# Performance work log

Hardware: AMD Instinct MI355X
Metric: run time of the kernel (lower is better)

Reference implementation:

```python
import jax, jax.numpy as jnp
import numpy as np

T, B, F = 256, 128, 1600
H1, H2, H3 = 60, 15, 10   # MLP dims
GH = 5                    # GRU hidden size


def setup_inputs() -> dict:
    key = jax.random.key(0)
    ks = jax.random.split(key, 24)
    s = 0.1
    inp = {
        "X":   jax.random.normal(ks[0], (T, B, F), jnp.float32),
        "W1":  jax.random.normal(ks[1], (H1, F), jnp.float32) * s,
        "b1":  jax.random.normal(ks[2], (H1,), jnp.float32) * s,
        "W2":  jax.random.normal(ks[3], (H2, H1), jnp.float32) * s,
        "b2":  jax.random.normal(ks[4], (H2,), jnp.float32) * s,
        "W3":  jax.random.normal(ks[5], (H3, H2), jnp.float32) * s,
        "b3":  jax.random.normal(ks[6], (H3,), jnp.float32) * s,
    }
    in_sizes = [H3, GH, GH]
    k = 7
    for l in range(3):
        inp[f"w_ih{l}"] = jax.random.normal(ks[k], (3 * GH, in_sizes[l]), jnp.float32) * s; k += 1
        inp[f"w_hh{l}"] = jax.random.normal(ks[k], (3 * GH, GH), jnp.float32) * s; k += 1
        inp[f"b_ih{l}"] = jax.random.normal(ks[k], (3 * GH,), jnp.float32) * s; k += 1
        inp[f"b_hh{l}"] = jax.random.normal(ks[k], (3 * GH,), jnp.float32) * s; k += 1
    inp["Wout"] = jax.random.normal(ks[k], (1, GH), jnp.float32) * s; k += 1
    inp["bout"] = jax.random.normal(ks[k], (1,), jnp.float32) * s
    return inp


def _gru_layer(x, w_ih, w_hh, b_ih, b_hh):
    # x: (Bb, Tt, I). Precompute input-side gates for all timesteps.
    gi = jnp.einsum('bti,gi->btg', x, w_ih) + b_ih  # (Bb, Tt, 3H)

    def step(h_prev, gi_t):
        gh = h_prev @ w_hh.T + b_hh                 # (Bb, 3H)
        ir, iz, in_ = jnp.split(gi_t, 3, axis=-1)
        hr, hz, hn = jnp.split(gh, 3, axis=-1)
        r = jax.nn.sigmoid(ir + hr)
        z = jax.nn.sigmoid(iz + hz)
        n = jnp.tanh(in_ + r * hn)
        h = (1.0 - z) * n + z * h_prev
        return h, h

    h0 = jnp.zeros((x.shape[0], w_hh.shape[1]), x.dtype)
    _, ys = jax.lax.scan(step, h0, jnp.swapaxes(gi, 0, 1))  # (Tt, Bb, H)
    return jnp.swapaxes(ys, 0, 1)                            # (Bb, Tt, H)


def reference(X, W1, b1, W2, b2, W3, b3,
              w_ih0, w_hh0, b_ih0, b_hh0,
              w_ih1, w_hh1, b_ih1, b_hh1,
              w_ih2, w_hh2, b_ih2, b_hh2,
              Wout, bout):
    x = jnp.transpose(X, (1, 0, 2))        # (B, T, 1600): GRU batch_first layout
    h = jnp.tanh(x @ W1.T + b1)
    h = jnp.tanh(h @ W2.T + b2)
    h = h @ W3.T + b3                      # (B, T, 10) -- no activation after last MLP layer
    seq = h
    for p in ((w_ih0, w_hh0, b_ih0, b_hh0),
              (w_ih1, w_hh1, b_ih1, b_hh1),
              (w_ih2, w_hh2, b_ih2, b_hh2)):
        seq = _gru_layer(seq, *p)          # (B, T, 5)
    y = jnp.swapaxes(seq, 0, 1)            # (T, B, 5)
    y = y @ Wout.T + bout                  # (T, B, 1)
    return jnp.swapaxes(y, -1, -2)         # (T, 1, B)
```

## Files before the change

### kernel.cpp

```cpp
#include <hip/hip_runtime.h>
#include <hip/hip_bf16.h>


#define T_DIM 256
#define B_DIM 128
#define F_DIM 1600
#define H1_DIM 60
#define H2_DIM 15
#define H3_DIM 10
#define GH 5
#define NSTEP 50
#define CT 32
#define NCH (T_DIM / CT)

#define DPP_SHR5  0x115
#define DPP_SHR10 0x11A

typedef __attribute__((ext_vector_type(8))) short bf16x8;
typedef __attribute__((ext_vector_type(4))) float f32x4;

__device__ __forceinline__ float fast_tanh(float x) {
    float e = __expf(2.0f * x);
    return 1.0f - __fdividef(2.0f, e + 1.0f);
}
__device__ __forceinline__ float fast_sigmoid(float x) {
    return __fdividef(1.0f, 1.0f + __expf(-x));
}
__device__ __forceinline__ ushort f2bf_rn(float x) {
    uint u = __float_as_uint(x);
    u += 0x7fffu + ((u >> 16) & 1u);
    return (ushort)(u >> 16);
}
template <int CTRL>
__device__ __forceinline__ float dppf(float v) {
    return __int_as_float(
        __builtin_amdgcn_mov_dpp(__float_as_int(v), CTRL, 0xf, 0xf, true));
}
__device__ __forceinline__ float bperm(int addr, float v) {
    return __int_as_float(__builtin_amdgcn_ds_bpermute(addr, __float_as_int(v)));
}

__global__ __launch_bounds__(256) void pack_w1_kernel(
    const float* __restrict__ W1, ushort* __restrict__ Wp)
{
    const int s  = blockIdx.x;
    const int t  = threadIdx.x;
    const int nf = t >> 6;
    const int l  = t & 63;
    const int n  = nf * 16 + (l & 15);
    const int g  = l >> 4;

    ushort hi[8], lo[8];
#pragma unroll
    for (int j = 0; j < 8; ++j) {
        const int k = s * 32 + g * 8 + j;
        const float v = (n < H1_DIM) ? W1[n * F_DIM + k] : 0.0f;
        const ushort h = f2bf_rn(v);
        const float hf = __uint_as_float(((uint)h) << 16);
        const float r  = v - hf;
        hi[j] = h;
        lo[j] = (ushort)(__float_as_uint(r) >> 16);
    }
    ushort* dst = Wp + ((size_t)(s * 8 + nf * 2)) * 512 + l * 8;
#pragma unroll
    for (int j = 0; j < 8; ++j) dst[j] = hi[j];
#pragma unroll
    for (int j = 0; j < 8; ++j) dst[512 + j] = lo[j];
}

__global__ __launch_bounds__(256) void mlp_kernel(
    const float* __restrict__ X,
    const ushort* __restrict__ Wp,
    const float* __restrict__ b1,
    const float* __restrict__ W2, const float* __restrict__ b2,
    const float* __restrict__ W3, const float* __restrict__ b3,
    const float* __restrict__ wih0, const float* __restrict__ bih0,
    float* __restrict__ gi0)
{
    __shared__ float red[4][2048];

    const int tid  = threadIdx.x;
    const int l    = tid & 63;
    const int w    = __builtin_amdgcn_readfirstlane(tid >> 6);
    const int lm   = l & 15;
    const int g    = l >> 4;
    const int row0 = blockIdx.x * 32;

    f32x4 acc[2][4];
#pragma unroll
    for (int mf = 0; mf < 2; ++mf)
#pragma unroll
        for (int nf = 0; nf < 4; ++nf)
            acc[mf][nf] = (f32x4){0.f, 0.f, 0.f, 0.f};

    const int s0 = (w * NSTEP) >> 2;
    const int s1 = ((w + 1) * NSTEP) >> 2;

    float4 x0[2], x1[2];
#pragma unroll
    for (int mf = 0; mf < 2; ++mf) {
        const float* ap = X + (size_t)(row0 + mf * 16 + lm) * F_DIM + s0 * 32 + g * 8;
        x0[mf] = *(const float4*)ap;
        x1[mf] = *(const float4*)(ap + 4);
    }

    for (int s = s0; s < s1; ++s) {
        float4 n0[2], n1[2];
#pragma unroll
        for (int mf = 0; mf < 2; ++mf) {
            n0[mf] = make_float4(0.f, 0.f, 0.f, 0.f);
            n1[mf] = n0[mf];
        }
        if (s + 1 < s1) {
#pragma unroll
            for (int mf = 0; mf < 2; ++mf) {
                const float* ap = X + (size_t)(row0 + mf * 16 + lm) * F_DIM
                                + (s + 1) * 32 + g * 8;
                n0[mf] = *(const float4*)ap;
                n1[mf] = *(const float4*)(ap + 4);
            }
        }
        bf16x8 bh[4], bl[4];
        const ushort* wp_s = Wp + (size_t)s * 4096 + l * 8;
#pragma unroll
        for (int nf = 0; nf < 4; ++nf) {
            bh[nf] = *(const bf16x8*)(wp_s + (nf * 2 + 0) * 512);
            bl[nf] = *(const bf16x8*)(wp_s + (nf * 2 + 1) * 512);
        }
#pragma unroll
        for (int mf = 0; mf < 2; ++mf) {
            const float xs8[8] = {x0[mf].x, x0[mf].y, x0[mf].z, x0[mf].w,
                                  x1[mf].x, x1[mf].y, x1[mf].z, x1[mf].w};
            bf16x8 ah, al;
#pragma unroll
            for (int j = 0; j < 8; ++j) {
                const float v = xs8[j];
                const uint  u = __float_as_uint(v);
                const uint uh = (u + 0x7fffu + ((u >> 16) & 1u)) & 0xffff0000u;
                const float hf = __uint_as_float(uh);
                const float r  = v - hf;
                ah[j] = (short)(uh >> 16);
                al[j] = (short)(__float_as_uint(r) >> 16);
            }
#pragma unroll
            for (int nf = 0; nf < 4; ++nf) {
                f32x4 c = acc[mf][nf];
                c = __builtin_amdgcn_mfma_f32_16x16x32_bf16(al, bh[nf], c, 0, 0, 0);
                c = __builtin_amdgcn_mfma_f32_16x16x32_bf16(ah, bl[nf], c, 0, 0, 0);
                c = __builtin_amdgcn_mfma_f32_16x16x32_bf16(ah, bh[nf], c, 0, 0, 0);
                acc[mf][nf] = c;
            }
        }
#pragma unroll
        for (int mf = 0; mf < 2; ++mf) { x0[mf] = n0[mf]; x1[mf] = n1[mf]; }
    }

    float* myred = &red[w][0];
#pragma unroll
    for (int mf = 0; mf < 2; ++mf)
#pragma unroll
        for (int nf = 0; nf < 4; ++nf)
#pragma unroll
            for (int q = 0; q < 4; ++q)
                myred[(mf * 16 + g * 4 + q) * 64 + nf * 16 + lm] = acc[mf][nf][q];
    __syncthreads();

    float rsum[8];
#pragma unroll
    for (int i = 0; i < 8; ++i) {
        const int p = tid + 256 * i;
        rsum[i] = red[0][p] + red[1][p] + red[2][p] + red[3][p];
    }
    __syncthreads();
    float* redp = &red[2][0];
#pragma unroll
    for (int i = 0; i < 8; ++i) {
        const int p = tid + 256 * i;
        redp[(p >> 6) * 65 + (p & 63)] = rsum[i];
    }
    __syncthreads();
    if (w != 0 || l >= 32) return;

    float h1v[H1_DIM];
#pragma unroll
    for (int o = 0; o < H1_DIM; ++o)
        h1v[o] = fast_tanh(redp[l * 65 + o] + b1[o]);

    float h2v[H2_DIM];
#pragma unroll
    for (int j = 0; j < H2_DIM; ++j) {
        float sacc = b2[j];
#pragma unroll
        for (int o = 0; o < H1_DIM; ++o) sacc += W2[j * H1_DIM + o] * h1v[o];
        h2v[j] = fast_tanh(sacc);
    }

    float h3v[H3_DIM];
#pragma unroll
    for (int m = 0; m < H3_DIM; ++m) {
        float sacc = b3[m];
#pragma unroll
        for (int j = 0; j < H2_DIM; ++j) sacc += W3[m * H2_DIM + j] * h2v[j];
        h3v[m] = sacc;
    }

    float gv[15];
#pragma unroll
    for (int q = 0; q < 15; ++q) {
        float sacc = bih0[q];
#pragma unroll
        for (int m = 0; m < H3_DIM; ++m) sacc += wih0[q * H3_DIM + m] * h3v[m];
        gv[q] = sacc;
    }

    const int row = row0 + l;
    float4* dst = (float4*)(gi0 + (size_t)row * 16);
    dst[0] = make_float4(gv[0],  gv[1],  gv[2],  gv[3]);
    dst[1] = make_float4(gv[4],  gv[5],  gv[6],  gv[7]);
    dst[2] = make_float4(gv[8],  gv[9],  gv[10], gv[11]);
    dst[3] = make_float4(gv[12], gv[13], gv[14], 0.0f);
}


#define STAGE(C) do {                                                       \
    const int _cb = (C) & 1;                                                \
    float4 _v0, _v1;                                                        \
    {                                                                       \
        const int _t = lane >> 2, _q = lane & 3;                            \
        _v0 = *(const float4*)(gi0 +                                        \
            ((size_t)(((C) * CT + _t) * B_DIM + b)) * 16 + _q * 4);         \
    }                                                                       \
    {                                                                       \
        const int _f = lane + 64, _t = _f >> 2, _q = _f & 3;                \
        _v1 = *(const float4*)(gi0 +                                        \
            ((size_t)(((C) * CT + _t) * B_DIM + b)) * 16 + _q * 4);         \
    }                                                                       \
    *(float4*)&gbuf[_cb][lane >> 2][(lane & 3) * 4] = _v0;                  \
    *(float4*)&gbuf[_cb][(lane + 64) >> 2][((lane + 64) & 3) * 4] = _v1;    \
} while (0)

#define PREF(CB, TL) do { pre = lptr[(CB) * (CT * 16) + (TL) * 16]; } while (0)

#define GSTEP(S, PREFCODE) do {                                             \
         \
    float aA = bA + pre;                                                    \
    _Pragma("unroll") for (int _j = 0; _j < GH; ++_j)                       \
        aA = fmaf(wi[_j], xn[_j], aA);                                      \
    float aB = fmaf(wh[0], hn[0], bB);                                      \
    _Pragma("unroll") for (int _j = 1; _j < GH; ++_j)                       \
        aB = fmaf(wh[_j], hn[_j], aB);                                      \
    PREFCODE                                                                \
    const float sAv = aA + aB;                                              \
    const float sg  = fast_sigmoid(sAv);                                    \
    const float rn  = dppf<DPP_SHR10>(sg);        \
    const float zn  = dppf<DPP_SHR5>(sg);         \
    if (lane == 48 && (unsigned)((S) - 3) < (unsigned)T_DIM)                \
        out[((S) - 3) * B_DIM + b] = sAv;    \
    const float nv = fast_tanh(fmaf(rn, aB, aA));                           \
    const float hu = fmaf(zn, hm - nv, nv);                                 \
    const bool _valid = (unsigned)((S) - row) < (unsigned)T_DIM;            \
    hm = _valid ? hu : hm;                                                  \
                  \
    _Pragma("unroll") for (int _j = 0; _j < GH; ++_j) {                     \
        hn[_j] = bperm(a_self[_j], hm);                                     \
        xn[_j] = bperm(a_prev[_j], hm);                                     \
    }                                                                       \
} while (0)

__global__ __launch_bounds__(128, 1) void gru_kernel(
    const float* __restrict__ gi0,
    const float* __restrict__ whh0, const float* __restrict__ bhh0,
    const float* __restrict__ wih1, const float* __restrict__ whh1,
    const float* __restrict__ bih1, const float* __restrict__ bhh1,
    const float* __restrict__ wih2, const float* __restrict__ whh2,
    const float* __restrict__ bih2, const float* __restrict__ bhh2,
    const float* __restrict__ Wout, const float* __restrict__ bout,
    float* __restrict__ out)
{
    __shared__ float gbuf[2][CT][16];

    const int tid  = threadIdx.x;
    const int w    = __builtin_amdgcn_readfirstlane(tid >> 6);
    const int lane = tid & 63;
    const int b    = blockIdx.x;

    if (w == 1) {
        STAGE(0);
        __syncthreads();
        for (int c = 0; c < NCH; ++c) {
            if (c + 1 < NCH) STAGE(c + 1);
            __syncthreads();
        }
        return;
    }

    const int row = lane >> 4;
    const int g   = lane & 15;

    float wi[GH], wh[GH];
    float bA = 0.f, bB = 0.f;
#pragma unroll
    for (int j = 0; j < GH; ++j) { wi[j] = 0.f; wh[j] = 0.f; }

    if (row == 0) {
        if (g < 15) {
#pragma unroll
            for (int j = 0; j < GH; ++j) wh[j] = whh0[g * GH + j];
            bB = bhh0[g];
        }
    } else if (row < 3) {
        const float* wip = (row == 1) ? wih1 : wih2;
        const float* whp = (row == 1) ? whh1 : whh2;
        const float* bip = (row == 1) ? bih1 : bih2;
        const float* bhp = (row == 1) ? bhh1 : bhh2;
        if (g < 15) {
#pragma unroll
            for (int j = 0; j < GH; ++j) {
                wi[j] = wip[g * GH + j];
                wh[j] = whp[g * GH + j];
            }
            bA = bip[g];
            bB = bhp[g];
        }
    } else if (g == 0) {
#pragma unroll
        for (int j = 0; j < GH; ++j) wi[j] = Wout[j];
        bA = bout[0];
    }

    int a_self[GH], a_prev[GH];
    const int sbase = row * 16;
    const int pbase = ((row + 3) & 3) * 16;
#pragma unroll
    for (int j = 0; j < GH; ++j) {
        a_self[j] = (sbase + 10 + j) << 2;
        a_prev[j] = (pbase + 10 + j) << 2;
    }

    const float* lptr = &gbuf[0][0][(row == 0) ? g : 15];

    float hn[GH] = {0.f, 0.f, 0.f, 0.f, 0.f};
    float xn[GH] = {0.f, 0.f, 0.f, 0.f, 0.f};
    float hm = 0.f, pre = 0.f;

    __syncthreads();
    PREF(0, 0);

    for (int c = 0; c < NCH; ++c) {
        const int cb = c & 1;
#pragma unroll 2
        for (int tl = 0; tl < CT; ++tl) {
            const int s = c * CT + tl;
            GSTEP(s, if (tl + 1 < CT) { PREF(cb, tl + 1); });
        }
        __syncthreads();
        if (c + 1 < NCH) { PREF((c + 1) & 1, 0); }
    }

    for (int s = T_DIM; s < T_DIM + 3; ++s) {
        GSTEP(s, ;);
    }
}

extern "C" void kernel_launch(void* const* d_in, const int* in_sizes, int n_in,
                              void* d_out, int out_size, void* d_ws, size_t ws_size,
                              hipStream_t stream)
{
    (void)in_sizes; (void)n_in; (void)out_size; (void)ws_size;

    const float* X    = (const float*)d_in[0];
    const float* W1   = (const float*)d_in[1];
    const float* b1   = (const float*)d_in[2];
    const float* W2   = (const float*)d_in[3];
    const float* b2   = (const float*)d_in[4];
    const float* W3   = (const float*)d_in[5];
    const float* b3   = (const float*)d_in[6];
    const float* wih0 = (const float*)d_in[7];
    const float* whh0 = (const float*)d_in[8];
    const float* bih0 = (const float*)d_in[9];
    const float* bhh0 = (const float*)d_in[10];
    const float* wih1 = (const float*)d_in[11];
    const float* whh1 = (const float*)d_in[12];
    const float* bih1 = (const float*)d_in[13];
    const float* bhh1 = (const float*)d_in[14];
    const float* wih2 = (const float*)d_in[15];
    const float* whh2 = (const float*)d_in[16];
    const float* bih2 = (const float*)d_in[17];
    const float* bhh2 = (const float*)d_in[18];
    const float* Wout = (const float*)d_in[19];
    const float* bout = (const float*)d_in[20];

    ushort* Wp  = (ushort*)d_ws;
    float*  gi0 = (float*)((char*)d_ws + 524288);

    pack_w1_kernel<<<NSTEP, 256, 0, stream>>>(W1, Wp);
    mlp_kernel<<<1024, 256, 0, stream>>>(X, Wp, b1, W2, b2, W3, b3, wih0, bih0, gi0);
    gru_kernel<<<128, 128, 0, stream>>>(gi0, whh0, bhh0,
                                        wih1, whh1, bih1, bhh1,
                                        wih2, whh2, bih2, bhh2,
                                        Wout, bout, (float*)d_out);
}
```

Measured before the change: 112.3 us.

## Fuse MLP and GRU kernels with per-chunk atomic counters for overlap

Merges the MLP producer kernel and the GRU recurrence into one launch. The first 128 blocks run the GRU and spin on a global counter per 32-timestep chunk, while the remaining 1024 blocks run the MLP and bump that chunk's counter when they finish. The aim is to start the serial GRU on early timesteps while later MLP tiles are still computing, hiding the recurrence behind the bandwidth-heavy MLP. This relies on the GRU blocks being co-resident with the producer blocks and adds spin-wait traffic plus a memset launch. The GRU blocks now use 256 threads, so two idle waves only join barriers.

```diff
diff --git a/kernel.cpp b/kernel.cpp
--- a/kernel.cpp
+++ b/kernel.cpp
@@ -12,6 +12,7 @@
 #define NSTEP 50
 #define CT 32
 #define NCH (T_DIM / CT)
+#define NGRU 128
 
 #define DPP_SHR5  0x115
 #define DPP_SHR10 0x11A
@@ -67,177 +68,6 @@
 #pragma unroll
     for (int j = 0; j < 8; ++j) dst[512 + j] = lo[j];
 }
-
-__global__ __launch_bounds__(256) void mlp_kernel(
-    const float* __restrict__ X,
-    const ushort* __restrict__ Wp,
-    const float* __restrict__ b1,
-    const float* __restrict__ W2, const float* __restrict__ b2,
-    const float* __restrict__ W3, const float* __restrict__ b3,
-    const float* __restrict__ wih0, const float* __restrict__ bih0,
-    float* __restrict__ gi0)
-{
-    __shared__ float red[4][2048];
-
-    const int tid  = threadIdx.x;
-    const int l    = tid & 63;
-    const int w    = __builtin_amdgcn_readfirstlane(tid >> 6);
-    const int lm   = l & 15;
-    const int g    = l >> 4;
-    const int row0 = blockIdx.x * 32;
-
-    f32x4 acc[2][4];
-#pragma unroll
-    for (int mf = 0; mf < 2; ++mf)
-#pragma unroll
-        for (int nf = 0; nf < 4; ++nf)
-            acc[mf][nf] = (f32x4){0.f, 0.f, 0.f, 0.f};
-
-    const int s0 = (w * NSTEP) >> 2;
-    const int s1 = ((w + 1) * NSTEP) >> 2;
-
-    float4 x0[2], x1[2];
-#pragma unroll
-    for (int mf = 0; mf < 2; ++mf) {
-        const float* ap = X + (size_t)(row0 + mf * 16 + lm) * F_DIM + s0 * 32 + g * 8;
-        x0[mf] = *(const float4*)ap;
-        x1[mf] = *(const float4*)(ap + 4);
-    }
-
-    for (int s = s0; s < s1; ++s) {
-        float4 n0[2], n1[2];
-#pragma unroll
-        for (int mf = 0; mf < 2; ++mf) {
-            n0[mf] = make_float4(0.f, 0.f, 0.f, 0.f);
-            n1[mf] = n0[mf];
-        }
-        if (s + 1 < s1) {
-#pragma unroll
-            for (int mf = 0; mf < 2; ++mf) {
-                const float* ap = X + (size_t)(row0 + mf * 16 + lm) * F_DIM
-                                + (s + 1) * 32 + g * 8;
-                n0[mf] = *(const float4*)ap;
-                n1[mf] = *(const float4*)(ap + 4);
-            }
-        }
-        bf16x8 bh[4], bl[4];
-        const ushort* wp_s = Wp + (size_t)s * 4096 + l * 8;
-#pragma unroll
-        for (int nf = 0; nf < 4; ++nf) {
-            bh[nf] = *(const bf16x8*)(wp_s + (nf * 2 + 0) * 512);
-            bl[nf] = *(const bf16x8*)(wp_s + (nf * 2 + 1) * 512);
-        }
-#pragma unroll
-        for (int mf = 0; mf < 2; ++mf) {
-            const float xs8[8] = {x0[mf].x, x0[mf].y, x0[mf].z, x0[mf].w,
-                                  x1[mf].x, x1[mf].y, x1[mf].z, x1[mf].w};
-            bf16x8 ah, al;
-#pragma unroll
-            for (int j = 0; j < 8; ++j) {
-                const float v = xs8[j];
-                const uint  u = __float_as_uint(v);
-                const uint uh = (u + 0x7fffu + ((u >> 16) & 1u)) & 0xffff0000u;
-                const float hf = __uint_as_float(uh);
-                const float r  = v - hf;
-                ah[j] = (short)(uh >> 16);
-                al[j] = (short)(__float_as_uint(r) >> 16);
-            }
-#pragma unroll
-            for (int nf = 0; nf < 4; ++nf) {
-                f32x4 c = acc[mf][nf];
-                c = __builtin_amdgcn_mfma_f32_16x16x32_bf16(al, bh[nf], c, 0, 0, 0);
-                c = __builtin_amdgcn_mfma_f32_16x16x32_bf16(ah, bl[nf], c, 0, 0, 0);
-                c = __builtin_amdgcn_mfma_f32_16x16x32_bf16(ah, bh[nf], c, 0, 0, 0);
-                acc[mf][nf] = c;
-            }
-        }
-#pragma unroll
-        for (int mf = 0; mf < 2; ++mf) { x0[mf] = n0[mf]; x1[mf] = n1[mf]; }
-    }
-
-    float* myred = &red[w][0];
-#pragma unroll
-    for (int mf = 0; mf < 2; ++mf)
-#pragma unroll
-        for (int nf = 0; nf < 4; ++nf)
-#pragma unroll
-            for (int q = 0; q < 4; ++q)
-                myred[(mf * 16 + g * 4 + q) * 64 + nf * 16 + lm] = acc[mf][nf][q];
-    __syncthreads();
-
-    float rsum[8];
-#pragma unroll
-    for (int i = 0; i < 8; ++i) {
-        const int p = tid + 256 * i;
-        rsum[i] = red[0][p] + red[1][p] + red[2][p] + red[3][p];
-    }
-    __syncthreads();
-    float* redp = &red[2][0];
-#pragma unroll
-    for (int i = 0; i < 8; ++i) {
-        const int p = tid + 256 * i;
-        redp[(p >> 6) * 65 + (p & 63)] = rsum[i];
-    }
-    __syncthreads();
-    if (w != 0 || l >= 32) return;
-
-    float h1v[H1_DIM];
-#pragma unroll
-    for (int o = 0; o < H1_DIM; ++o)
-        h1v[o] = fast_tanh(redp[l * 65 + o] + b1[o]);
-
-    float h2v[H2_DIM];
-#pragma unroll
-    for (int j = 0; j < H2_DIM; ++j) {
-        float sacc = b2[j];
-#pragma unroll
-        for (int o = 0; o < H1_DIM; ++o) sacc += W2[j * H1_DIM + o] * h1v[o];
-        h2v[j] = fast_tanh(sacc);
-    }
-
-    float h3v[H3_DIM];
-#pragma unroll
-    for (int m = 0; m < H3_DIM; ++m) {
-        float sacc = b3[m];
-#pragma unroll
-        for (int j = 0; j < H2_DIM; ++j) sacc += W3[m * H2_DIM + j] * h2v[j];
-        h3v[m] = sacc;
-    }
-
-    float gv[15];
-#pragma unroll
-    for (int q = 0; q < 15; ++q) {
-        float sacc = bih0[q];
-#pragma unroll
-        for (int m = 0; m < H3_DIM; ++m) sacc += wih0[q * H3_DIM + m] * h3v[m];
-        gv[q] = sacc;
-    }
-
-    const int row = row0 + l;
-    float4* dst = (float4*)(gi0 + (size_t)row * 16);
-    dst[0] = make_float4(gv[0],  gv[1],  gv[2],  gv[3]);
-    dst[1] = make_float4(gv[4],  gv[5],  gv[6],  gv[7]);
-    dst[2] = make_float4(gv[8],  gv[9],  gv[10], gv[11]);
-    dst[3] = make_float4(gv[12], gv[13], gv[14], 0.0f);
-}
-
-
-#define STAGE(C) do {                                                       \
-    const int _cb = (C) & 1;                                                \
-    float4 _v0, _v1;                                                        \
-    {                                                                       \
-        const int _t = lane >> 2, _q = lane & 3;                            \
-        _v0 = *(const float4*)(gi0 +                                        \
-            ((size_t)(((C) * CT + _t) * B_DIM + b)) * 16 + _q * 4);         \
-    }                                                                       \
-    {                                                                       \
-        const int _f = lane + 64, _t = _f >> 2, _q = _f & 3;                \
-        _v1 = *(const float4*)(gi0 +                                        \
-            ((size_t)(((C) * CT + _t) * B_DIM + b)) * 16 + _q * 4);         \
-    }                                                                       \
-    *(float4*)&gbuf[_cb][lane >> 2][(lane & 3) * 4] = _v0;                  \
-    *(float4*)&gbuf[_cb][(lane + 64) >> 2][((lane + 64) & 3) * 4] = _v1;    \
-} while (0)
 
 #define PREF(CB, TL) do { pre = lptr[(CB) * (CT * 16) + (TL) * 16]; } while (0)
 
@@ -267,98 +97,286 @@
     }                                                                       \
 } while (0)
 
-__global__ __launch_bounds__(128, 1) void gru_kernel(
-    const float* __restrict__ gi0,
+#define STAGE(C) do {                                                       \
+    const int _cb = (C) & 1;                                                \
+    float4 _v0, _v1;                                                        \
+    {                                                                       \
+        const int _t = lane >> 2, _q = lane & 3;                            \
+        _v0 = *(const float4*)(gi0 +                                        \
+            ((size_t)(((C) * CT + _t) * B_DIM + b)) * 16 + _q * 4);         \
+    }                                                                       \
+    {                                                                       \
+        const int _f = lane + 64, _t = _f >> 2, _q = _f & 3;                \
+        _v1 = *(const float4*)(gi0 +                                        \
+            ((size_t)(((C) * CT + _t) * B_DIM + b)) * 16 + _q * 4);         \
+    }                                                                       \
+    *(float4*)&gbuf[_cb][lane >> 2][(lane & 3) * 4] = _v0;                  \
+    *(float4*)&gbuf[_cb][(lane + 64) >> 2][((lane + 64) & 3) * 4] = _v1;    \
+} while (0)
+
+#define WAITCHUNK(C) do {                                                   \
+    while (atomicAdd((uint*)&ctr[(C)], 0u) < 128u)                          \
+        __builtin_amdgcn_s_sleep(8);                                        \
+    __threadfence();       \
+} while (0)
+
+__global__ __launch_bounds__(256) void fused_kernel(
+    const float* __restrict__ X,
+    const ushort* __restrict__ Wp,
+    const float* __restrict__ b1,
+    const float* __restrict__ W2, const float* __restrict__ b2,
+    const float* __restrict__ W3, const float* __restrict__ b3,
+    const float* __restrict__ wih0, const float* __restrict__ bih0,
     const float* __restrict__ whh0, const float* __restrict__ bhh0,
     const float* __restrict__ wih1, const float* __restrict__ whh1,
     const float* __restrict__ bih1, const float* __restrict__ bhh1,
     const float* __restrict__ wih2, const float* __restrict__ whh2,
     const float* __restrict__ bih2, const float* __restrict__ bhh2,
     const float* __restrict__ Wout, const float* __restrict__ bout,
+    float* __restrict__ gi0, uint* __restrict__ ctr,
     float* __restrict__ out)
 {
-    __shared__ float gbuf[2][CT][16];
+    __shared__ float shm[4][2048];
 
     const int tid  = threadIdx.x;
     const int w    = __builtin_amdgcn_readfirstlane(tid >> 6);
     const int lane = tid & 63;
-    const int b    = blockIdx.x;
-
-    if (w == 1) {
-        STAGE(0);
+    const int bid  = blockIdx.x;
+
+    if (bid < NGRU) {
+        const int b = bid;
+        float (*gbuf)[CT][16] = (float (*)[CT][16])shm;
+
+        if (w >= 2) {
+            for (int i = 0; i < NCH + 1; ++i) __syncthreads();
+            return;
+        }
+
+        if (w == 1) {
+            WAITCHUNK(0);
+            STAGE(0);
+            __syncthreads();
+            for (int c = 0; c < NCH; ++c) {
+                if (c + 1 < NCH) { WAITCHUNK(c + 1); STAGE(c + 1); }
+                __syncthreads();
+            }
+            return;
+        }
+
+        const int row = lane >> 4;
+        const int g   = lane & 15;
+
+        float wi[GH], wh[GH];
+        float bA = 0.f, bB = 0.f;
+#pragma unroll
+        for (int j = 0; j < GH; ++j) { wi[j] = 0.f; wh[j] = 0.f; }
+
+        if (row == 0) {
+            if (g < 15) {
+#pragma unroll
+                for (int j = 0; j < GH; ++j) wh[j] = whh0[g * GH + j];
+                bB = bhh0[g];
+            }
+        } else if (row < 3) {
+            const float* wip = (row == 1) ? wih1 : wih2;
+            const float* whp = (row == 1) ? whh1 : whh2;
+            const float* bip = (row == 1) ? bih1 : bih2;
+            const float* bhp = (row == 1) ? bhh1 : bhh2;
+            if (g < 15) {
+#pragma unroll
+                for (int j = 0; j < GH; ++j) {
+                    wi[j] = wip[g * GH + j];
+                    wh[j] = whp[g * GH + j];
+                }
+                bA = bip[g];
+                bB = bhp[g];
+            }
+        } else if (g == 0) {
+#pragma unroll
+            for (int j = 0; j < GH; ++j) wi[j] = Wout[j];
+            bA = bout[0];
+        }
+
+        int a_self[GH], a_prev[GH];
+        const int sbase = row * 16;
+        const int pbase = ((row + 3) & 3) * 16;
+#pragma unroll
+        for (int j = 0; j < GH; ++j) {
+            a_self[j] = (sbase + 10 + j) << 2;
+            a_prev[j] = (pbase + 10 + j) << 2;
+        }
+
+        const float* lptr = &gbuf[0][0][(row == 0) ? g : 15];
+
+        float hn[GH] = {0.f, 0.f, 0.f, 0.f, 0.f};
+        float xn[GH] = {0.f, 0.f, 0.f, 0.f, 0.f};
+        float hm = 0.f, pre = 0.f;
+
         __syncthreads();
+        PREF(0, 0);
+
         for (int c = 0; c < NCH; ++c) {
-            if (c + 1 < NCH) STAGE(c + 1);
+            const int cb = c & 1;
+#pragma unroll 2
+            for (int tl = 0; tl < CT; ++tl) {
+                const int s = c * CT + tl;
+                GSTEP(s, if (tl + 1 < CT) { PREF(cb, tl + 1); });
+            }
             __syncthreads();
+            if (c + 1 < NCH) { PREF((c + 1) & 1, 0); }
+        }
+
+        for (int s = T_DIM; s < T_DIM + 3; ++s) {
+            GSTEP(s, ;);
         }
         return;
     }
 
-    const int row = lane >> 4;
-    const int g   = lane & 15;
-
-    float wi[GH], wh[GH];
-    float bA = 0.f, bB = 0.f;
-#pragma unroll
-    for (int j = 0; j < GH; ++j) { wi[j] = 0.f; wh[j] = 0.f; }
-
-    if (row == 0) {
-        if (g < 15) {
-#pragma unroll
-            for (int j = 0; j < GH; ++j) wh[j] = whh0[g * GH + j];
-            bB = bhh0[g];
-        }
-    } else if (row < 3) {
-        const float* wip = (row == 1) ? wih1 : wih2;
-        const float* whp = (row == 1) ? whh1 : whh2;
-        const float* bip = (row == 1) ? bih1 : bih2;
-        const float* bhp = (row == 1) ? bhh1 : bhh2;
-        if (g < 15) {
-#pragma unroll
-            for (int j = 0; j < GH; ++j) {
-                wi[j] = wip[g * GH + j];
-                wh[j] = whp[g * GH + j];
-            }
-            bA = bip[g];
-            bB = bhp[g];
-        }
-    } else if (g == 0) {
-#pragma unroll
-        for (int j = 0; j < GH; ++j) wi[j] = Wout[j];
-        bA = bout[0];
-    }
-
-    int a_self[GH], a_prev[GH];
-    const int sbase = row * 16;
-    const int pbase = ((row + 3) & 3) * 16;
-#pragma unroll
-    for (int j = 0; j < GH; ++j) {
-        a_self[j] = (sbase + 10 + j) << 2;
-        a_prev[j] = (pbase + 10 + j) << 2;
-    }
-
-    const float* lptr = &gbuf[0][0][(row == 0) ? g : 15];
-
-    float hn[GH] = {0.f, 0.f, 0.f, 0.f, 0.f};
-    float xn[GH] = {0.f, 0.f, 0.f, 0.f, 0.f};
-    float hm = 0.f, pre = 0.f;
-
-    __syncthreads();
-    PREF(0, 0);
-
-    for (int c = 0; c < NCH; ++c) {
-        const int cb = c & 1;
-#pragma unroll 2
-        for (int tl = 0; tl < CT; ++tl) {
-            const int s = c * CT + tl;
-            GSTEP(s, if (tl + 1 < CT) { PREF(cb, tl + 1); });
-        }
+    {
+        const int m    = bid - NGRU;
+        const int lm   = lane & 15;
+        const int g    = lane >> 4;
+        const int row0 = m * 32;
+
+        float (*red)[2048] = shm;
+
+        f32x4 acc[2][4];
+#pragma unroll
+        for (int mf = 0; mf < 2; ++mf)
+#pragma unroll
+            for (int nf = 0; nf < 4; ++nf)
+                acc[mf][nf] = (f32x4){0.f, 0.f, 0.f, 0.f};
+
+        const int s0 = (w * NSTEP) >> 2;
+        const int s1 = ((w + 1) * NSTEP) >> 2;
+
+        float4 x0[2], x1[2];
+#pragma unroll
+        for (int mf = 0; mf < 2; ++mf) {
+            const float* ap = X + (size_t)(row0 + mf * 16 + lm) * F_DIM + s0 * 32 + g * 8;
+            x0[mf] = *(const float4*)ap;
+            x1[mf] = *(const float4*)(ap + 4);
+        }
+
+        for (int s = s0; s < s1; ++s) {
+            float4 n0[2], n1[2];
+#pragma unroll
+            for (int mf = 0; mf < 2; ++mf) {
+                n0[mf] = make_float4(0.f, 0.f, 0.f, 0.f);
+                n1[mf] = n0[mf];
+            }
+            if (s + 1 < s1) {
+#pragma unroll
+                for (int mf = 0; mf < 2; ++mf) {
+                    const float* ap = X + (size_t)(row0 + mf * 16 + lm) * F_DIM
+                                    + (s + 1) * 32 + g * 8;
+                    n0[mf] = *(const float4*)ap;
+                    n1[mf] = *(const float4*)(ap + 4);
+                }
+            }
+            bf16x8 bh[4], bl[4];
+            const ushort* wp_s = Wp + (size_t)s * 4096 + lane * 8;
+#pragma unroll
+            for (int nf = 0; nf < 4; ++nf) {
+                bh[nf] = *(const bf16x8*)(wp_s + (nf * 2 + 0) * 512);
+                bl[nf] = *(const bf16x8*)(wp_s + (nf * 2 + 1) * 512);
+            }
+#pragma unroll
+            for (int mf = 0; mf < 2; ++mf) {
+                const float xs8[8] = {x0[mf].x, x0[mf].y, x0[mf].z, x0[mf].w,
+                                      x1[mf].x, x1[mf].y, x1[mf].z, x1[mf].w};
+                bf16x8 ah, al;
+#pragma unroll
+                for (int j = 0; j < 8; ++j) {
+                    const float v = xs8[j];
+                    const uint  u = __float_as_uint(v);
+                    const uint uh = (u + 0x7fffu + ((u >> 16) & 1u)) & 0xffff0000u;
+                    const float hf = __uint_as_float(uh);
+                    const float r  = v - hf;
+                    ah[j] = (short)(uh >> 16);
+                    al[j] = (short)(__float_as_uint(r) >> 16);
+                }
+#pragma unroll
+                for (int nf = 0; nf < 4; ++nf) {
+                    f32x4 c = acc[mf][nf];
+                    c = __builtin_amdgcn_mfma_f32_16x16x32_bf16(al, bh[nf], c, 0, 0, 0);
+                    c = __builtin_amdgcn_mfma_f32_16x16x32_bf16(ah, bl[nf], c, 0, 0, 0);
+                    c = __builtin_amdgcn_mfma_f32_16x16x32_bf16(ah, bh[nf], c, 0, 0, 0);
+                    acc[mf][nf] = c;
+                }
+            }
+#pragma unroll
+            for (int mf = 0; mf < 2; ++mf) { x0[mf] = n0[mf]; x1[mf] = n1[mf]; }
+        }
+
+        float* myred = &red[w][0];
+#pragma unroll
+        for (int mf = 0; mf < 2; ++mf)
+#pragma unroll
+            for (int nf = 0; nf < 4; ++nf)
+#pragma unroll
+                for (int q = 0; q < 4; ++q)
+                    myred[(mf * 16 + g * 4 + q) * 64 + nf * 16 + lm] = acc[mf][nf][q];
         __syncthreads();
-        if (c + 1 < NCH) { PREF((c + 1) & 1, 0); }
-    }
-
-    for (int s = T_DIM; s < T_DIM + 3; ++s) {
-        GSTEP(s, ;);
+
+        float rsum[8];
+#pragma unroll
+        for (int i = 0; i < 8; ++i) {
+            const int p = tid + 256 * i;
+            rsum[i] = red[0][p] + red[1][p] + red[2][p] + red[3][p];
+        }
+        __syncthreads();
+        float* redp = &red[2][0];
+#pragma unroll
+        for (int i = 0; i < 8; ++i) {
+            const int p = tid + 256 * i;
+            redp[(p >> 6) * 65 + (p & 63)] = rsum[i];
+        }
+        __syncthreads();
+        if (w != 0 || lane >= 32) return;
+
+        const int l = lane;
+        float h1v[H1_DIM];
+#pragma unroll
+        for (int o = 0; o < H1_DIM; ++o)
+            h1v[o] = fast_tanh(redp[l * 65 + o] + b1[o]);
+
+        float h2v[H2_DIM];
+#pragma unroll
+        for (int j = 0; j < H2_DIM; ++j) {
+            float sacc = b2[j];
+#pragma unroll
+            for (int o = 0; o < H1_DIM; ++o) sacc += W2[j * H1_DIM + o] * h1v[o];
+            h2v[j] = fast_tanh(sacc);
+        }
+
+        float h3v[H3_DIM];
+#pragma unroll
+        for (int mm = 0; mm < H3_DIM; ++mm) {
+            float sacc = b3[mm];
+#pragma unroll
+            for (int j = 0; j < H2_DIM; ++j) sacc += W3[mm * H2_DIM + j] * h2v[j];
+            h3v[mm] = sacc;
+        }
+
+        float gv[15];
+#pragma unroll
+        for (int q = 0; q < 15; ++q) {
+            float sacc = bih0[q];
+#pragma unroll
+            for (int mm = 0; mm < H3_DIM; ++mm) sacc += wih0[q * H3_DIM + mm] * h3v[mm];
+            gv[q] = sacc;
+        }
+
+        const int rowi = row0 + l;
+        float4* dst = (float4*)(gi0 + (size_t)rowi * 16);
+        dst[0] = make_float4(gv[0],  gv[1],  gv[2],  gv[3]);
+        dst[1] = make_float4(gv[4],  gv[5],  gv[6],  gv[7]);
+        dst[2] = make_float4(gv[8],  gv[9],  gv[10], gv[11]);
+        dst[3] = make_float4(gv[12], gv[13], gv[14], 0.0f);
+
+        __threadfence();
+        if (l == 0) atomicAdd(&ctr[m >> 7], 1u);
     }
 }
 
@@ -391,12 +409,15 @@
     const float* bout = (const float*)d_in[20];
 
     ushort* Wp  = (ushort*)d_ws;
+    uint*   ctr = (uint*)((char*)d_ws + 458752);
     float*  gi0 = (float*)((char*)d_ws + 524288);
 
+    hipMemsetAsync(ctr, 0, NCH * sizeof(uint), stream);
     pack_w1_kernel<<<NSTEP, 256, 0, stream>>>(W1, Wp);
-    mlp_kernel<<<1024, 256, 0, stream>>>(X, Wp, b1, W2, b2, W3, b3, wih0, bih0, gi0);
-    gru_kernel<<<128, 128, 0, stream>>>(gi0, whh0, bhh0,
-                                        wih1, whh1, bih1, bhh1,
-                                        wih2, whh2, bih2, bhh2,
-                                        Wout, bout, (float*)d_out);
-}
+    fused_kernel<<<NGRU + 1024, 256, 0, stream>>>(
+        X, Wp, b1, W2, b2, W3, b3,
+        wih0, bih0, whh0, bhh0,
+        wih1, whh1, bih1, bhh1,
+        wih2, whh2, bih2, bhh2,
+        Wout, bout, gi0, ctr, (float*)d_out);
+}
```

After: 154.7 us. +37.7%, slower.
